# Optimization experiments

Hardware: AMD Instinct MI355X
Metric: run time of the kernel (lower is better)

The kernel has to match this reference:

```python
import jax, jax.numpy as jnp
import numpy as np
from jax import lax

NPOINT = 1024
RADIUS = 0.2
NSAMPLE = 32
BN_EPS = 1e-5


def farthest_point_sample(xyz, npoint):
    # xyz: (B, N, 3). Deterministic start at index 0 (torch uses randint).
    B, N, _ = xyz.shape

    def step(carry, _):
        distance, farthest = carry
        centroid = jnp.take_along_axis(xyz, farthest[:, None, None], axis=1)  # (B,1,3)
        d = jnp.sum((xyz - centroid) ** 2, axis=-1)  # (B,N)
        distance = jnp.minimum(distance, d)
        return (distance, jnp.argmax(distance, axis=-1).astype(jnp.int32)), farthest

    init = (jnp.full((B, N), 1e10, xyz.dtype), jnp.zeros((B,), jnp.int32))
    _, idxs = lax.scan(step, init, None, length=npoint)  # (npoint, B)
    return jnp.transpose(idxs)  # (B, npoint)


def square_distance(src, dst):
    # src: (B,S,3), dst: (B,N,3) -> (B,S,N) squared distances
    d = -2.0 * jnp.einsum('bsc,bnc->bsn', src, dst)
    d = d + jnp.sum(src ** 2, axis=-1)[:, :, None]
    d = d + jnp.sum(dst ** 2, axis=-1)[:, None, :]
    return d


def query_ball_point(radius, nsample, xyz, new_xyz):
    B, N, _ = xyz.shape
    S = new_xyz.shape[1]
    sqrdists = square_distance(new_xyz, xyz)  # (B,S,N)
    idx = jnp.broadcast_to(jnp.arange(N, dtype=jnp.int32), (B, S, N))
    idx = jnp.where(sqrdists > radius ** 2, N, idx)
    idx = jnp.sort(idx, axis=-1)[:, :, :nsample]  # (B,S,K)
    first = idx[:, :, :1]
    return jnp.where(idx == N, first, idx)


# batched gather: points (B,N,C), idx (B,...) -> (B,...,C)
_gather = jax.vmap(lambda p, i: p[i])


def bn_relu(x, gamma, beta):
    # training-mode BatchNorm2d over (B, C, S, K): stats over axes (0,2,3)
    m = jnp.mean(x, axis=(0, 2, 3), keepdims=True)
    v = jnp.var(x, axis=(0, 2, 3), keepdims=True)
    y = (x - m) * lax.rsqrt(v + BN_EPS)
    return jax.nn.relu(y * gamma[None, :, None, None] + beta[None, :, None, None])


def reference(xyz, points, W0, b0, g0, be0, W1, b1, g1, be1, W2, b2, g2, be2):
    # xyz: (B,3,N), points: (B,C,N)
    xyz_t = jnp.transpose(xyz, (0, 2, 1))      # (B,N,3)
    pts_t = jnp.transpose(points, (0, 2, 1))   # (B,N,C)

    fps_idx = farthest_point_sample(xyz_t, NPOINT)          # (B,S)
    new_xyz = _gather(xyz_t, fps_idx)                        # (B,S,3)
    group_idx = query_ball_point(RADIUS, NSAMPLE, xyz_t, new_xyz)  # (B,S,K)

    grouped_xyz = _gather(xyz_t, group_idx) - new_xyz[:, :, None, :]  # (B,S,K,3)
    grouped_pts = _gather(pts_t, group_idx)                           # (B,S,K,C)
    feat = jnp.concatenate([grouped_xyz, grouped_pts], axis=-1)      # (B,S,K,C+3)

    x = jnp.transpose(feat, (0, 3, 1, 2))  # (B, C+3, S, K)
    for W, b, g, be in ((W0, b0, g0, be0), (W1, b1, g1, be1), (W2, b2, g2, be2)):
        x = bn_relu(jnp.einsum('bcsk,oc->bosk', x, W) + b[None, :, None, None], g, be)
    new_points = jnp.max(x, axis=-1)  # (B, C_out, S)

    return jnp.transpose(new_xyz, (0, 2, 1)), new_points


def setup_inputs() -> dict:
    key = jax.random.key(0)
    ks = jax.random.split(key, 8)
    B, C_in, N = 16, 6, 4096
    inp = {
        'xyz': jax.random.uniform(ks[0], (B, 3, N), dtype=jnp.float32),
        'points': jax.random.normal(ks[1], (B, C_in, N), dtype=jnp.float32),
        'W0': 0.1 * jax.random.normal(ks[2], (32, C_in + 3), dtype=jnp.float32),
        'b0': 0.1 * jax.random.normal(ks[3], (32,), dtype=jnp.float32),
        'g0': jnp.ones((32,), jnp.float32),
        'be0': jnp.zeros((32,), jnp.float32),
        'W1': 0.1 * jax.random.normal(ks[4], (32, 32), dtype=jnp.float32),
        'b1': 0.1 * jax.random.normal(ks[5], (32,), dtype=jnp.float32),
        'g1': jnp.ones((32,), jnp.float32),
        'be1': jnp.zeros((32,), jnp.float32),
        'W2': 0.1 * jax.random.normal(ks[6], (64, 32), dtype=jnp.float32),
        'b2': 0.1 * jax.random.normal(ks[7], (64,), dtype=jnp.float32),
        'g2': jnp.ones((64,), jnp.float32),
        'be2': jnp.zeros((64,), jnp.float32),
    }
    return inp
```

## Files before the change

kernel.cpp:

```cpp
#include <hip/hip_runtime.h>

#define BATCH   16
#define NPTS    4096
#define NPOINT  1024
#define NSAMPLE 32
#define NSITES  (BATCH*NPOINT*NSAMPLE)

typedef float f32x2 __attribute__((ext_vector_type(2)));


__device__ __forceinline__ float wave_max_bcast(float x) {
    int v = __float_as_int(x);
    int t;
    t = __builtin_amdgcn_update_dpp(v, v, 0x111, 0xf, 0xf, false);
    v = __float_as_int(fmaxf(__int_as_float(v), __int_as_float(t)));
    t = __builtin_amdgcn_update_dpp(v, v, 0x112, 0xf, 0xf, false);
    v = __float_as_int(fmaxf(__int_as_float(v), __int_as_float(t)));
    t = __builtin_amdgcn_update_dpp(v, v, 0x114, 0xf, 0xf, false);
    v = __float_as_int(fmaxf(__int_as_float(v), __int_as_float(t)));
    t = __builtin_amdgcn_update_dpp(v, v, 0x118, 0xf, 0xf, false);
    v = __float_as_int(fmaxf(__int_as_float(v), __int_as_float(t)));
    t = __builtin_amdgcn_update_dpp(v, v, 0x142, 0xa, 0xf, false);
    v = __float_as_int(fmaxf(__int_as_float(v), __int_as_float(t)));
    t = __builtin_amdgcn_update_dpp(v, v, 0x143, 0xc, 0xf, false);
    v = __float_as_int(fmaxf(__int_as_float(v), __int_as_float(t)));
    return __int_as_float(__builtin_amdgcn_readlane(v, 63));
}

__global__ __launch_bounds__(512, 1) void fps_kernel(
    const float* __restrict__ xyz,
    float* __restrict__ nxyz,
    float* __restrict__ out0)
{
    __shared__ float sx[NPTS], sy[NPTS], sz[NPTS];
    __shared__ int   s_sel[NPOINT];
    __shared__ unsigned long long redK[2][8];

    const int b = blockIdx.x;
    const int t = threadIdx.x;
    const int wave = t >> 6, lane = t & 63;
    const float* xb = xyz + (size_t)b * 3 * NPTS;

    for (int i = t; i < NPTS; i += 512) {
        sx[i] = xb[i]; sy[i] = xb[NPTS+i]; sz[i] = xb[2*NPTS+i];
    }
    __syncthreads();

    const int base = t * 8;
    f32x2 px[4], py[4], pz[4], dd[4];
    #pragma unroll
    for (int k = 0; k < 4; ++k) {
        px[k] = (f32x2){ sx[base+2*k], sx[base+2*k+1] };
        py[k] = (f32x2){ sy[base+2*k], sy[base+2*k+1] };
        pz[k] = (f32x2){ sz[base+2*k], sz[base+2*k+1] };
        dd[k] = (f32x2){ 1e10f, 1e10f };
    }

    int far = 0;
    float cx = sx[0], cy = sy[0], cz = sz[0];
    for (int it = 0; it < NPOINT; ++it) {
        if (t == 0) s_sel[it] = far;
        const f32x2 vcx = (f32x2){cx, cx};
        const f32x2 vcy = (f32x2){cy, cy};
        const f32x2 vcz = (f32x2){cz, cz};
        #pragma unroll
        for (int k = 0; k < 4; ++k) {
            const f32x2 dx = px[k] - vcx;
            const f32x2 dy = py[k] - vcy;
            const f32x2 dz = pz[k] - vcz;
            const f32x2 s  = (dx*dx + dy*dy) + dz*dz;
            dd[k].x = fminf(dd[k].x, s.x);
            dd[k].y = fminf(dd[k].y, s.y);
        }
        const float d0 = dd[0].x, d1 = dd[0].y, d2 = dd[1].x, d3 = dd[1].y;
        const float d4 = dd[2].x, d5 = dd[2].y, d6 = dd[3].x, d7 = dd[3].y;
        float tv0, tv1, tv2, tv3; int ti0, ti1, ti2, ti3;
        { bool c = d1 > d0; tv0 = c ? d1 : d0; ti0 = c ? 1 : 0; }
        { bool c = d3 > d2; tv1 = c ? d3 : d2; ti1 = c ? 3 : 2; }
        { bool c = d5 > d4; tv2 = c ? d5 : d4; ti2 = c ? 5 : 4; }
        { bool c = d7 > d6; tv3 = c ? d7 : d6; ti3 = c ? 7 : 6; }
        float nv0, nv1; int ni0, ni1;
        { bool c = tv1 > tv0; nv0 = c ? tv1 : tv0; ni0 = c ? ti1 : ti0; }
        { bool c = tv3 > tv2; nv1 = c ? tv3 : tv2; ni1 = c ? ti3 : ti2; }
        float bm; int bj;
        { bool c = nv1 > nv0; bm = c ? nv1 : nv0; bj = c ? ni1 : ni0; }
        const float M = wave_max_bcast(bm);
        const unsigned long long mask = __ballot(bm == M);
        const int wl = __ffsll((long long)mask) - 1;
        const int par = it & 1;
        if (lane == wl) {
            const unsigned idxg = (unsigned)(base + bj);
            redK[par][wave] = ((unsigned long long)__float_as_uint(M) << 32)
                              | (unsigned)(~idxg);
        }
        __syncthreads();
        const unsigned long long k0 = redK[par][0], k1 = redK[par][1];
        const unsigned long long k2 = redK[par][2], k3 = redK[par][3];
        const unsigned long long k4 = redK[par][4], k5 = redK[par][5];
        const unsigned long long k6 = redK[par][6], k7 = redK[par][7];
        const unsigned long long a0 = (k1 > k0) ? k1 : k0;
        const unsigned long long a1 = (k3 > k2) ? k3 : k2;
        const unsigned long long a2 = (k5 > k4) ? k5 : k4;
        const unsigned long long a3 = (k7 > k6) ? k7 : k6;
        const unsigned long long b0_ = (a1 > a0) ? a1 : a0;
        const unsigned long long b1_ = (a3 > a2) ? a3 : a2;
        const unsigned long long km  = (b1_ > b0_) ? b1_ : b0_;
        far = (int)((~(unsigned)km) & (NPTS-1));
        cx = sx[far]; cy = sy[far]; cz = sz[far];
    }
    __syncthreads();
    for (int s = t; s < NPOINT; s += 512) {
        const int id = s_sel[s];
        const float x = sx[id], y = sy[id], z = sz[id];
        nxyz[((size_t)b*NPOINT + s)*3 + 0] = x;
        nxyz[((size_t)b*NPOINT + s)*3 + 1] = y;
        nxyz[((size_t)b*NPOINT + s)*3 + 2] = z;
        out0[(size_t)b*3*NPOINT + 0*NPOINT + s] = x;
        out0[(size_t)b*3*NPOINT + 1*NPOINT + s] = y;
        out0[(size_t)b*3*NPOINT + 2*NPOINT + s] = z;
    }
}

__global__ __launch_bounds__(256) void ball_kernel(
    const float* __restrict__ xyz, const float* __restrict__ nxyz,
    int* __restrict__ gidx)
{
    __shared__ float sx[NPTS], sy[NPTS], sz[NPTS];
    const int b  = blockIdx.x >> 4;
    const int sg = blockIdx.x & 15;
    const int t = threadIdx.x;
    const int wave = t >> 6, lane = t & 63;
    const float* xb = xyz + (size_t)b * 3 * NPTS;
    for (int i = t; i < NPTS; i += 256) {
        sx[i] = xb[i]; sy[i] = xb[NPTS+i]; sz[i] = xb[2*NPTS+i];
    }
    __syncthreads();
    const unsigned long long lt = (1ull << lane) - 1ull;

    for (int q = wave; q < 64; q += 4) {
        const int s = sg*64 + q;
        const size_t bs = (size_t)b*NPOINT + s;
        const float cx = nxyz[bs*3+0], cy = nxyz[bs*3+1], cz = nxyz[bs*3+2];
        const float ss = __fadd_rn(__fadd_rn(__fmul_rn(cx,cx), __fmul_rn(cy,cy)),
                                   __fmul_rn(cz,cz));
        int* out = gidx + bs*NSAMPLE;
        int cnt = 0;
        int firstIdx = NPTS;
        for (int ch = 0; ch < NPTS/64 && cnt < NSAMPLE; ++ch) {
            const int pi = ch*64 + lane;
            const float qx = sx[pi], qy = sy[pi], qz = sz[pi];
            const float dot = fmaf(cz, qz, fmaf(cy, qy, __fmul_rn(cx, qx)));
            const float sn  = __fadd_rn(__fadd_rn(__fmul_rn(qx,qx), __fmul_rn(qy,qy)),
                                        __fmul_rn(qz,qz));
            const float d   = __fadd_rn(__fadd_rn(__fmul_rn(-2.0f,dot), ss), sn);
            const bool pred = !(d > 0.04f);
            const unsigned long long m = __ballot(pred);
            if (pred) {
                const int pos = cnt + __popcll(m & lt);
                if (pos == 0) firstIdx = pi;
                if (pos < NSAMPLE) out[pos] = pi;
            }
            cnt += (int)__popcll(m);
        }
        if (cnt < NSAMPLE) {
            #pragma unroll
            for (int off = 32; off >= 1; off >>= 1) {
                const int oi = __shfl_xor(firstIdx, off);
                firstIdx = (oi < firstIdx) ? oi : firstIdx;
            }
            for (int p = cnt + lane; p < NSAMPLE; p += 64) out[p] = firstIdx;
        }
    }
}

__device__ __forceinline__ void gather_feat(
    const float* __restrict__ xyz, const float* __restrict__ pts,
    const int* __restrict__ gidx, const float* __restrict__ nxyz,
    int v, float4 f[9])
{
    const int site = v * 4;
    const int bs = site >> 5;
    const int b  = bs >> 10;
    const int4 idx = *reinterpret_cast<const int4*>(gidx + site);
    const float* xb = xyz + (size_t)b*3*NPTS;
    const float* pb = pts + (size_t)b*6*NPTS;
    const float cx = nxyz[(size_t)bs*3+0];
    const float cy = nxyz[(size_t)bs*3+1];
    const float cz = nxyz[(size_t)bs*3+2];
    f[0] = make_float4(xb[idx.x]-cx, xb[idx.y]-cx, xb[idx.z]-cx, xb[idx.w]-cx);
    f[1] = make_float4(xb[NPTS+idx.x]-cy, xb[NPTS+idx.y]-cy, xb[NPTS+idx.z]-cy, xb[NPTS+idx.w]-cy);
    f[2] = make_float4(xb[2*NPTS+idx.x]-cz, xb[2*NPTS+idx.y]-cz, xb[2*NPTS+idx.z]-cz, xb[2*NPTS+idx.w]-cz);
    #pragma unroll
    for (int c = 0; c < 6; ++c)
        f[3+c] = make_float4(pb[c*NPTS+idx.x], pb[c*NPTS+idx.y], pb[c*NPTS+idx.z], pb[c*NPTS+idx.w]);
}

__global__ __launch_bounds__(256) void conv0s_kernel(
    const float* __restrict__ xyz, const float* __restrict__ pts,
    const int* __restrict__ gidx, const float* __restrict__ nxyz,
    const float* __restrict__ W, const float* __restrict__ bias,
    float* __restrict__ xout, float* __restrict__ psum, float* __restrict__ psq)
{
    const int t = threadIdx.x;
    const int v = blockIdx.x*256 + t;
    const int site = v * 4;
    float4 f[9];
    gather_feat(xyz, pts, gidx, nxyz, v, f);
    float acc[32], accq[32];
    #pragma unroll
    for (int o = 0; o < 32; ++o) {
        const float bb = bias[o];
        float4 y = make_float4(bb,bb,bb,bb);
        #pragma unroll
        for (int c = 0; c < 9; ++c) {
            const float w = W[o*9+c];
            y.x = fmaf(w, f[c].x, y.x); y.y = fmaf(w, f[c].y, y.y);
            y.z = fmaf(w, f[c].z, y.z); y.w = fmaf(w, f[c].w, y.w);
        }
        *reinterpret_cast<float4*>(xout + (size_t)o*NSITES + site) = y;
        acc[o]  = (y.x + y.y) + (y.z + y.w);
        accq[o] = (y.x*y.x + y.y*y.y) + (y.z*y.z + y.w*y.w);
    }
    __shared__ float ls[4][32], lq[4][32];
    const int wave = t>>6, lane = t&63;
    #pragma unroll
    for (int o = 0; o < 32; ++o) {
        float s1 = acc[o], q1 = accq[o];
        #pragma unroll
        for (int off = 32; off >= 1; off >>= 1) {
            s1 += __shfl_xor(s1, off);
            q1 += __shfl_xor(q1, off);
        }
        if (lane == 0) { ls[wave][o] = s1; lq[wave][o] = q1; }
    }
    __syncthreads();
    if (t < 32) {
        psum[blockIdx.x*64 + t] = (ls[0][t]+ls[1][t]) + (ls[2][t]+ls[3][t]);
        psq [blockIdx.x*64 + t] = (lq[0][t]+lq[1][t]) + (lq[2][t]+lq[3][t]);
    }
}

__global__ void fold_kernel(
    const float* __restrict__ g, const float* __restrict__ be,
    const float* __restrict__ psum, const float* __restrict__ psq,
    float* __restrict__ aff, int Cout)
{
    __shared__ float ss[4][64], qq[4][64];
    const int t = threadIdx.x;
    const int ch = t & 63, part = t >> 6;
    float s = 0.f, q = 0.f;
    for (int i = part; i < 512; i += 4) {
        s += psum[i*64 + ch];
        q += psq [i*64 + ch];
    }
    ss[part][ch] = s; qq[part][ch] = q;
    __syncthreads();
    if (t < Cout) {
        s = (ss[0][t]+ss[1][t]) + (ss[2][t]+ss[3][t]);
        q = (qq[0][t]+qq[1][t]) + (qq[2][t]+qq[3][t]);
        const float invn = 1.0f / (float)NSITES;
        const float m = s * invn;
        float v2 = fmaxf(q * invn - m*m, 0.f);
        const float a = g[t] * rsqrtf(v2 + 1e-5f);
        aff[t]      = a;
        aff[64 + t] = fmaf(-m, a, be[t]);
    }
}

__global__ __launch_bounds__(256) void conv1s_kernel(
    const float* x, float* xout,
    const float* __restrict__ aff, const float* __restrict__ W,
    const float* __restrict__ bias,
    float* __restrict__ psum, float* __restrict__ psq)
{
    const int t = threadIdx.x;
    const int v = blockIdx.x*256 + t;
    const int site = v * 4;
    float4 in[32];
    #pragma unroll
    for (int c = 0; c < 32; ++c) {
        float4 r = *reinterpret_cast<const float4*>(x + (size_t)c*NSITES + site);
        const float a = aff[c], cc = aff[64 + c];
        in[c].x = fmaxf(fmaf(a, r.x, cc), 0.f);
        in[c].y = fmaxf(fmaf(a, r.y, cc), 0.f);
        in[c].z = fmaxf(fmaf(a, r.z, cc), 0.f);
        in[c].w = fmaxf(fmaf(a, r.w, cc), 0.f);
    }
    float acc[32], accq[32];
    #pragma unroll
    for (int o = 0; o < 32; ++o) {
        const float bb = bias[o];
        float4 y = make_float4(bb,bb,bb,bb);
        #pragma unroll
        for (int c = 0; c < 32; ++c) {
            const float w = W[o*32+c];
            y.x = fmaf(w, in[c].x, y.x); y.y = fmaf(w, in[c].y, y.y);
            y.z = fmaf(w, in[c].z, y.z); y.w = fmaf(w, in[c].w, y.w);
        }
        *reinterpret_cast<float4*>(xout + (size_t)o*NSITES + site) = y;
        acc[o]  = (y.x + y.y) + (y.z + y.w);
        accq[o] = (y.x*y.x + y.y*y.y) + (y.z*y.z + y.w*y.w);
    }
    __shared__ float ls[4][32], lq[4][32];
    const int wave = t>>6, lane = t&63;
    #pragma unroll
    for (int o = 0; o < 32; ++o) {
        float s1 = acc[o], q1 = accq[o];
        #pragma unroll
        for (int off = 32; off >= 1; off >>= 1) {
            s1 += __shfl_xor(s1, off);
            q1 += __shfl_xor(q1, off);
        }
        if (lane == 0) { ls[wave][o] = s1; lq[wave][o] = q1; }
    }
    __syncthreads();
    if (t < 32) {
        psum[blockIdx.x*64 + t] = (ls[0][t]+ls[1][t]) + (ls[2][t]+ls[3][t]);
        psq [blockIdx.x*64 + t] = (lq[0][t]+lq[1][t]) + (lq[2][t]+lq[3][t]);
    }
}

__global__ __launch_bounds__(512, 1) void conv2stats_kernel(
    const float* __restrict__ x, const float* __restrict__ aff,
    const float* __restrict__ W, const float* __restrict__ bias,
    float* __restrict__ psum, float* __restrict__ psq)
{
    const int t = threadIdx.x;
    const int v = blockIdx.x*512 + t;
    const int site = v * 2;
    float2 in[32];
    #pragma unroll
    for (int c = 0; c < 32; ++c) {
        const float2 r = *reinterpret_cast<const float2*>(x + (size_t)c*NSITES + site);
        const float a = aff[c], cc = aff[64 + c];
        in[c].x = fmaxf(fmaf(a, r.x, cc), 0.f);
        in[c].y = fmaxf(fmaf(a, r.y, cc), 0.f);
    }
    float acc[64], accq[64];
    #pragma unroll
    for (int o = 0; o < 64; ++o) {
        const float bb = bias[o];
        float yx = bb, yy = bb;
        #pragma unroll
        for (int c = 0; c < 32; ++c) {
            const float w = W[o*32+c];
            yx = fmaf(w, in[c].x, yx);
            yy = fmaf(w, in[c].y, yy);
        }
        acc[o]  = yx + yy;
        accq[o] = yx*yx + yy*yy;
    }
    __shared__ float ls[8][64], lq[8][64];
    const int wave = t>>6, lane = t&63;
    #pragma unroll
    for (int o = 0; o < 64; ++o) {
        float s1 = acc[o], q1 = accq[o];
        #pragma unroll
        for (int off = 32; off >= 1; off >>= 1) {
            s1 += __shfl_xor(s1, off);
            q1 += __shfl_xor(q1, off);
        }
        if (lane == 0) { ls[wave][o] = s1; lq[wave][o] = q1; }
    }
    __syncthreads();
    if (t < 64) {
        psum[blockIdx.x*64 + t] = ((ls[0][t]+ls[1][t]) + (ls[2][t]+ls[3][t]))
                                + ((ls[4][t]+ls[5][t]) + (ls[6][t]+ls[7][t]));
        psq [blockIdx.x*64 + t] = ((lq[0][t]+lq[1][t]) + (lq[2][t]+lq[3][t]))
                                + ((lq[4][t]+lq[5][t]) + (lq[6][t]+lq[7][t]));
    }
}

__global__ __launch_bounds__(256) void conv2max_kernel(
    const float* __restrict__ x, const float* __restrict__ aff1,
    const float* __restrict__ aff2, const float* __restrict__ W,
    const float* __restrict__ bias, float* __restrict__ outp)
{
    const int gt = blockIdx.x*256 + threadIdx.x;
    const int wv = gt >> 6;
    const int lane = gt & 63;
    const int base = wv * 64;
    float in[32];
    #pragma unroll
    for (int c = 0; c < 32; ++c) {
        const float r = x[(size_t)c*NSITES + base + lane];
        in[c] = fmaxf(fmaf(aff1[c], r, aff1[64 + c]), 0.f);
    }
    const int bs = (base + lane) >> 5;
    const int b = bs >> 10, s = bs & 1023;
    float* dst = outp + (size_t)b*64*NPOINT + s;
    for (int o = 0; o < 64; ++o) {
        float z = bias[o];
        #pragma unroll
        for (int c = 0; c < 32; ++c)
            z = fmaf(W[o*32+c], in[c], z);
        float y = fmaxf(fmaf(aff2[o], z, aff2[64 + o]), 0.f);
        #pragma unroll
        for (int off = 16; off >= 1; off >>= 1)
            y = fmaxf(y, __shfl_xor(y, off));
        if ((lane & 31) == 0)
            dst[(size_t)o*NPOINT] = y;
    }
}

extern "C" void kernel_launch(void* const* d_in, const int* in_sizes, int n_in,
                              void* d_out, int out_size, void* d_ws, size_t ws_size,
                              hipStream_t stream) {
    (void)in_sizes; (void)n_in; (void)out_size; (void)ws_size;
    const float* xyz = (const float*)d_in[0];
    const float* pts = (const float*)d_in[1];
    const float* W0  = (const float*)d_in[2];
    const float* b0  = (const float*)d_in[3];
    const float* g0  = (const float*)d_in[4];
    const float* be0 = (const float*)d_in[5];
    const float* W1  = (const float*)d_in[6];
    const float* b1  = (const float*)d_in[7];
    const float* g1  = (const float*)d_in[8];
    const float* be1 = (const float*)d_in[9];
    const float* W2  = (const float*)d_in[10];
    const float* b2  = (const float*)d_in[11];
    const float* g2  = (const float*)d_in[12];
    const float* be2 = (const float*)d_in[13];
    float* out = (float*)d_out;
    char* ws = (char*)d_ws;
    float* nxyz = (float*)(ws + 0);
    int*   gidx = (int*)  (ws + 196608);
    float* psum = (float*)(ws + 2293760);
    float* psq  = (float*)(ws + 2424832);
    float* aff0 = (float*)(ws + 2555904);
    float* aff1 = (float*)(ws + 2556416);
    float* aff2 = (float*)(ws + 2556928);
    float* xbuf = (float*)(ws + 2557440);

    fps_kernel <<<16,  512, 0, stream>>>(xyz, nxyz, out);
    ball_kernel<<<256, 256, 0, stream>>>(xyz, nxyz, gidx);

    conv0s_kernel<<<512, 256, 0, stream>>>(xyz, pts, gidx, nxyz, W0, b0,
                                           xbuf, psum, psq);
    fold_kernel<<<1, 256, 0, stream>>>(g0, be0, psum, psq, aff0, 32);

    conv1s_kernel<<<512, 256, 0, stream>>>(xbuf, xbuf, aff0, W1, b1, psum, psq);
    fold_kernel<<<1, 256, 0, stream>>>(g1, be1, psum, psq, aff1, 32);

    conv2stats_kernel<<<512, 512, 0, stream>>>(xbuf, aff1, W2, b2, psum, psq);
    fold_kernel<<<1, 256, 0, stream>>>(g2, be2, psum, psq, aff2, 64);

    conv2max_kernel<<<2048, 256, 0, stream>>>(xbuf, aff1, aff2, W2, b2,
                                              out + 49152);
}
```

Before: 982.3 us.

## Pack two FPS batches per 1024-thread block sharing barriers

The farthest-point-sampling kernel now runs two batch elements in one 1024-thread block, each half using its own shared-memory arrays, instead of one batch per 512-thread block. This halves the number of blocks from 16 to 8 and doubles shared-memory use per block. Both groups now share every __syncthreads, so each iteration's barrier spans 16 waves and the slower half sets the pace. Only 8 CUs are used, and it is unclear why this would speed up a latency-bound serial loop.

```diff
diff --git a/kernel.cpp b/kernel.cpp
--- a/kernel.cpp
+++ b/kernel.cpp
@@ -27,22 +27,25 @@
     return __int_as_float(__builtin_amdgcn_readlane(v, 63));
 }
 
-__global__ __launch_bounds__(512, 1) void fps_kernel(
+__global__ __launch_bounds__(1024, 1) void fps_kernel(
     const float* __restrict__ xyz,
     float* __restrict__ nxyz,
     float* __restrict__ out0)
 {
-    __shared__ float sx[NPTS], sy[NPTS], sz[NPTS];
-    __shared__ int   s_sel[NPOINT];
-    __shared__ unsigned long long redK[2][8];
-
-    const int b = blockIdx.x;
-    const int t = threadIdx.x;
-    const int wave = t >> 6, lane = t & 63;
+    __shared__ float sx[2][NPTS], sy[2][NPTS], sz[2][NPTS];
+    __shared__ int   s_sel[2][NPOINT];
+    __shared__ unsigned long long redK[2][2][8];
+
+    const int tt = threadIdx.x;
+    const int g  = tt >> 9;
+    const int t  = tt & 511;
+    const int wave = t >> 6;
+    const int lane = tt & 63;
+    const int b = blockIdx.x * 2 + g;
     const float* xb = xyz + (size_t)b * 3 * NPTS;
 
     for (int i = t; i < NPTS; i += 512) {
-        sx[i] = xb[i]; sy[i] = xb[NPTS+i]; sz[i] = xb[2*NPTS+i];
+        sx[g][i] = xb[i]; sy[g][i] = xb[NPTS+i]; sz[g][i] = xb[2*NPTS+i];
     }
     __syncthreads();
 
@@ -50,16 +53,16 @@
     f32x2 px[4], py[4], pz[4], dd[4];
     #pragma unroll
     for (int k = 0; k < 4; ++k) {
-        px[k] = (f32x2){ sx[base+2*k], sx[base+2*k+1] };
-        py[k] = (f32x2){ sy[base+2*k], sy[base+2*k+1] };
-        pz[k] = (f32x2){ sz[base+2*k], sz[base+2*k+1] };
+        px[k] = (f32x2){ sx[g][base+2*k], sx[g][base+2*k+1] };
+        py[k] = (f32x2){ sy[g][base+2*k], sy[g][base+2*k+1] };
+        pz[k] = (f32x2){ sz[g][base+2*k], sz[g][base+2*k+1] };
         dd[k] = (f32x2){ 1e10f, 1e10f };
     }
 
     int far = 0;
-    float cx = sx[0], cy = sy[0], cz = sz[0];
+    float cx = sx[g][0], cy = sy[g][0], cz = sz[g][0];
     for (int it = 0; it < NPOINT; ++it) {
-        if (t == 0) s_sel[it] = far;
+        if (t == 0) s_sel[g][it] = far;
         const f32x2 vcx = (f32x2){cx, cx};
         const f32x2 vcy = (f32x2){cy, cy};
         const f32x2 vcz = (f32x2){cz, cz};
@@ -90,14 +93,14 @@
         const int par = it & 1;
         if (lane == wl) {
             const unsigned idxg = (unsigned)(base + bj);
-            redK[par][wave] = ((unsigned long long)__float_as_uint(M) << 32)
-                              | (unsigned)(~idxg);
+            redK[g][par][wave] = ((unsigned long long)__float_as_uint(M) << 32)
+                                 | (unsigned)(~idxg);
         }
         __syncthreads();
-        const unsigned long long k0 = redK[par][0], k1 = redK[par][1];
-        const unsigned long long k2 = redK[par][2], k3 = redK[par][3];
-        const unsigned long long k4 = redK[par][4], k5 = redK[par][5];
-        const unsigned long long k6 = redK[par][6], k7 = redK[par][7];
+        const unsigned long long k0 = redK[g][par][0], k1 = redK[g][par][1];
+        const unsigned long long k2 = redK[g][par][2], k3 = redK[g][par][3];
+        const unsigned long long k4 = redK[g][par][4], k5 = redK[g][par][5];
+        const unsigned long long k6 = redK[g][par][6], k7 = redK[g][par][7];
         const unsigned long long a0 = (k1 > k0) ? k1 : k0;
         const unsigned long long a1 = (k3 > k2) ? k3 : k2;
         const unsigned long long a2 = (k5 > k4) ? k5 : k4;
@@ -106,12 +109,12 @@
         const unsigned long long b1_ = (a3 > a2) ? a3 : a2;
         const unsigned long long km  = (b1_ > b0_) ? b1_ : b0_;
         far = (int)((~(unsigned)km) & (NPTS-1));
-        cx = sx[far]; cy = sy[far]; cz = sz[far];
+        cx = sx[g][far]; cy = sy[g][far]; cz = sz[g][far];
     }
     __syncthreads();
     for (int s = t; s < NPOINT; s += 512) {
-        const int id = s_sel[s];
-        const float x = sx[id], y = sy[id], z = sz[id];
+        const int id = s_sel[g][s];
+        const float x = sx[g][id], y = sy[g][id], z = sz[g][id];
         nxyz[((size_t)b*NPOINT + s)*3 + 0] = x;
         nxyz[((size_t)b*NPOINT + s)*3 + 1] = y;
         nxyz[((size_t)b*NPOINT + s)*3 + 2] = z;
@@ -432,7 +435,7 @@
     float* aff2 = (float*)(ws + 2556928);
     float* xbuf = (float*)(ws + 2557440);
 
-    fps_kernel <<<16,  512, 0, stream>>>(xyz, nxyz, out);
+    fps_kernel <<<8,  1024, 0, stream>>>(xyz, nxyz, out);
     ball_kernel<<<256, 256, 0, stream>>>(xyz, nxyz, gidx);
 
     conv0s_kernel<<<512, 256, 0, stream>>>(xyz, pts, gidx, nxyz, W0, b0,
```

After: 1.291 ms. 1.31x slower.
